# Kernel optimization log

Hardware: AMD Instinct MI355X
Metric: run time of the kernel (lower is better)

## Reference

```python
import jax, jax.numpy as jnp
import numpy as np

B, N, E, H, F, L, S = 4, 384, 768, 32, 3072, 12, 512
D = E // H


def setup_inputs() -> dict:
    key = jax.random.key(0)
    ks = jax.random.split(key, 32)
    inp = {}
    # forward args
    inp['node_type'] = jax.random.randint(ks[0], (B, N, 1), 1, S + 1)  # table has S+1 rows; 0 = pad (unused)
    inp['node_input_feature'] = jax.random.normal(ks[1], (B, N, E), jnp.float32)
    inp['in_degree'] = jax.random.randint(ks[2], (B, N), 0, S)
    inp['out_degree'] = jax.random.randint(ks[3], (B, N), 0, S)
    inp['attn_bias'] = jax.random.normal(ks[4], (B, N, N), jnp.float32) * 0.1
    inp['spatial_pos'] = jax.random.randint(ks[5], (B, N, N), 0, S)
    # embedding tables (normal stddev 0.02, as in the flax module)
    inp['node_emb'] = jax.random.normal(ks[6], (S + 1, E), jnp.float32) * 0.02
    inp['in_deg_emb'] = jax.random.normal(ks[7], (S, E), jnp.float32) * 0.02
    inp['out_deg_emb'] = jax.random.normal(ks[8], (S, E), jnp.float32) * 0.02
    inp['sp_emb'] = jax.random.normal(ks[9], (S, H), jnp.float32) * 0.02
    inp['sp_emb_rev'] = jax.random.normal(ks[10], (S, H), jnp.float32) * 0.02
    # per-layer weights, stacked along leading L axis
    se, sf = 1.0 / np.sqrt(E), 1.0 / np.sqrt(F)
    inp['Wq'] = jax.random.normal(ks[11], (L, E, E), jnp.float32) * se
    inp['bq'] = jax.random.normal(ks[12], (L, E), jnp.float32) * se
    inp['Wk'] = jax.random.normal(ks[13], (L, E, E), jnp.float32) * se
    inp['bk'] = jax.random.normal(ks[14], (L, E), jnp.float32) * se
    inp['Wv'] = jax.random.normal(ks[15], (L, E, E), jnp.float32) * se
    inp['bv'] = jax.random.normal(ks[16], (L, E), jnp.float32) * se
    inp['Wo'] = jax.random.normal(ks[17], (L, E, E), jnp.float32) * se
    inp['bo'] = jnp.zeros((L, E), jnp.float32)
    inp['W1'] = jax.random.normal(ks[18], (L, E, F), jnp.float32) * se
    inp['b1'] = jax.random.normal(ks[19], (L, F), jnp.float32) * se
    inp['W2'] = jax.random.normal(ks[20], (L, F, E), jnp.float32) * sf
    inp['b2'] = jax.random.normal(ks[21], (L, E), jnp.float32) * sf
    inp['ln1_s'] = jnp.ones((L, E), jnp.float32)
    inp['ln1_b'] = jnp.zeros((L, E), jnp.float32)
    inp['ln2_s'] = jnp.ones((L, E), jnp.float32)
    inp['ln2_b'] = jnp.zeros((L, E), jnp.float32)
    return inp


def _layernorm(x, scale, bias, eps=1e-5):
    m = x.mean(-1, keepdims=True)
    v = ((x - m) ** 2).mean(-1, keepdims=True)
    return (x - m) / jnp.sqrt(v + eps) * scale + bias


def _encoder(node_type, node_input_feature, in_degree, out_degree, attn_bias, spatial_pos,
             node_emb, in_deg_emb, out_deg_emb, sp_emb, sp_emb_rev,
             Wq, bq, Wk, bk, Wv, bv, Wo, bo, W1, b1, W2, b2, ln1_s, ln1_b, ln2_s, ln2_b):
    nt = node_type[..., 0]                               # [B,N]
    padding_mask = nt == 0                               # [B,N]
    # node features: node_emb(node_type).sum(-2) + degree embeddings + input feature
    x = (node_emb[node_type].sum(axis=-2)
         + in_deg_emb[in_degree] + out_deg_emb[out_degree]
         + node_input_feature)                           # [B,N,E]
    # spatial attention bias: [B,N,N,H] -> [B,H,N,N], plus graph-level attn_bias
    sb = sp_emb[spatial_pos] + sp_emb_rev[jnp.transpose(spatial_pos, (0, 2, 1))]
    bias = jnp.transpose(sb, (0, 3, 1, 2)) + attn_bias[:, None]  # [B,H,N,N]

    x = jnp.transpose(x, (1, 0, 2))                      # [N,B,E]
    scaling = D ** (-0.5)
    neg_inf = jnp.float32(-jnp.inf)

    def layer(x, p):
        wq, bq_, wk, bk_, wv, bv_, wo, bo_, w1, b1_, w2, b2_, s1, t1, s2, t2 = p
        q = ((x @ wq) + bq_) * scaling                   # [N,B,E], bias scaled too (faithful)
        k = (x @ wk) + bk_
        v = (x @ wv) + bv_
        q = q.reshape(N, B, H, D)
        k = k.reshape(N, B, H, D)
        v = v.reshape(N, B, H, D)
        w = jnp.einsum('nbhd,mbhd->bhnm', q, k) + bias   # [B,H,N,N]
        w = jnp.where(padding_mask[:, None, None, :], neg_inf, w)
        probs = jax.nn.softmax(w.astype(jnp.float32), axis=-1).astype(x.dtype)
        a = jnp.einsum('bhnm,mbhd->nbhd', probs, v).reshape(N, B, E)
        a = a @ wo + bo_
        x = _layernorm(x + a, s1, t1)                    # post-LN
        h = jax.nn.gelu(x @ w1 + b1_)                    # approximate gelu (flax default)
        h = h @ w2 + b2_
        x = _layernorm(x + h, s2, t2)
        return x, None

    xs = (Wq, bq, Wk, bk, Wv, bv, Wo, bo, W1, b1, W2, b2, ln1_s, ln1_b, ln2_s, ln2_b)
    x, _ = jax.lax.scan(layer, x, xs)
    return x                                             # [N,B,E]


def reference(node_type, node_input_feature, in_degree, out_degree, attn_bias, spatial_pos,
              node_emb, in_deg_emb, out_deg_emb, sp_emb, sp_emb_rev,
              Wq, bq, Wk, bk, Wv, bv, Wo, bo, W1, b1, W2, b2, ln1_s, ln1_b, ln2_s, ln2_b):
    return _encoder(node_type, node_input_feature, in_degree, out_degree, attn_bias, spatial_pos,
                    node_emb, in_deg_emb, out_deg_emb, sp_emb, sp_emb_rev,
                    Wq, bq, Wk, bk, Wv, bv, Wo, bo, W1, b1, W2, b2, ln1_s, ln1_b, ln2_s, ln2_b)
```

## Files before the change

kernel.cpp:

```cpp
#include <hip/hip_runtime.h>
#include <hip/hip_bf16.h>

#define Bb 4
#define Nn 384
#define Ee 768
#define Hh 32
#define Ff 3072
#define Ll 12
#define Ss 512
#define Mm (Nn*Bb)

typedef __attribute__((ext_vector_type(8))) short bf16x8;
typedef __attribute__((ext_vector_type(4))) float f32x4;
typedef unsigned short u16;

__device__ __forceinline__ u16 f2b(float f) {
  union { float f; unsigned int i; } c; c.f = f;
  unsigned int x = c.i;
  return (u16)((x + 0x7fffu + ((x >> 16) & 1u)) >> 16);
}
__device__ __forceinline__ float b2f(u16 u) {
  union { unsigned int i; float f; } c; c.i = ((unsigned int)u) << 16; return c.f;
}
__device__ __forceinline__ unsigned pkcvt(float lo, float hi) {
  unsigned r;
  asm("v_cvt_pk_bf16_f32 %0, %1, %2" : "=v"(r) : "v"(lo), "v"(hi));
  return r;
}
__device__ __forceinline__ void gload_lds16(const void* g, void* l) {
  __builtin_amdgcn_global_load_lds((__attribute__((address_space(1))) void*)(g),
                                   (__attribute__((address_space(3))) void*)(l), 16, 0, 0);
}

__global__ __launch_bounds__(256) void embed_kernel(
    const int* __restrict__ node_type, const float* __restrict__ nif,
    const int* __restrict__ in_deg, const int* __restrict__ out_deg,
    const float* __restrict__ node_emb, const float* __restrict__ ind_emb,
    const float* __restrict__ outd_emb,
    float* __restrict__ x, u16* __restrict__ xb)
{
  const int r = blockIdx.x;
  const int n = r / Bb, b = r % Bb;
  const int nt  = node_type[b*Nn + n];
  const int idg = in_deg[b*Nn + n];
  const int odg = out_deg[b*Nn + n];
  for (int c = threadIdx.x; c < Ee; c += 256) {
    float val = node_emb[(size_t)nt*Ee + c] + ind_emb[(size_t)idg*Ee + c]
              + outd_emb[(size_t)odg*Ee + c] + nif[((size_t)b*Nn + n)*Ee + c];
    x[(size_t)r*Ee + c] = val;
    xb[(size_t)r*Ee + c] = f2b(val);
  }
}

__global__ void spT_kernel(const int* __restrict__ sp, int* __restrict__ spT)
{
  __shared__ int tile[32][33];
  const int b = blockIdx.z;
  const int n0 = blockIdx.y * 32, m0 = blockIdx.x * 32;
  const int tx = threadIdx.x, ty = threadIdx.y;
  for (int i = ty; i < 32; i += 8)
    tile[i][tx] = sp[((size_t)b*Nn + n0 + i)*Nn + m0 + tx];
  __syncthreads();
  for (int i = ty; i < 32; i += 8)
    spT[((size_t)b*Nn + m0 + i)*Nn + n0 + tx] = tile[tx][i];
}

__global__ __launch_bounds__(256) void bias_pre_kernel(
    const float* __restrict__ atb, const int* __restrict__ sp, const int* __restrict__ spT,
    const float* __restrict__ sp_emb, const float* __restrict__ sp_emb_rev,
    u16* __restrict__ biasb)
{
  __shared__ float spc[512], sprc[512];
  const int bx = blockIdx.x, h = blockIdx.y, b = blockIdx.z;
  const int t = threadIdx.x;
  for (int i = t; i < 512; i += 256) {
    spc[i]  = sp_emb[(size_t)i*Hh + h];
    sprc[i] = sp_emb_rev[(size_t)i*Hh + h];
  }
  __syncthreads();
  const int q = bx*16 + ((t >> 2) & 15);
  const size_t rowb = ((size_t)b*Nn + q)*Nn;
  u16* outb = biasb + (((size_t)(b*Hh + h)*24 + bx)*24)*256 + t;
  const int mbase = ((t >> 6) << 2) + (t & 3);
  for (int tt = 0; tt < 24; ++tt) {
    const int m = tt*16 + mbase;
    float v = atb[rowb + m] + spc[sp[rowb + m]] + sprc[spT[rowb + m]];
    outb[tt*256] = f2b(v);
  }
}

__global__ __launch_bounds__(256) void wconv_kernel(
    const float* __restrict__ Wq, const float* __restrict__ Wk, const float* __restrict__ Wv,
    const float* __restrict__ Wo, const float* __restrict__ W1, const float* __restrict__ W2,
    int layer0, u16* __restrict__ wTall, unsigned slotStride)
{
  __shared__ float tile[64][65];
  const int layer = layer0 + blockIdx.y;
  u16* slot = wTall + (size_t)blockIdx.y * slotStride;
  int tid = blockIdx.x;
  const float* src; u16* dst; int Ns, Ks;
  if (tid < 432)       { int seg = tid / 144; tid -= seg*144;
                         src = (seg==0?Wq:(seg==1?Wk:Wv)) + (size_t)layer*Ee*Ee;
                         dst = slot + (size_t)seg*589824; Ns = 768; Ks = 768; }
  else if (tid < 576)  { tid -= 432; src = Wo + (size_t)layer*Ee*Ee; dst = slot + 1769472; Ns = 768;  Ks = 768; }
  else if (tid < 1152) { tid -= 576; src = W1 + (size_t)layer*Ee*Ff; dst = slot + 2359296; Ns = 3072; Ks = 768; }
  else                 { tid -= 1152; src = W2 + (size_t)layer*Ff*Ee; dst = slot + 4718592; Ns = 768; Ks = 3072; }
  const int tc = Ns >> 6;
  const int tk = tid / tc, tn = tid % tc;
  const int t = threadIdx.x;
  #pragma unroll
  for (int i = 0; i < 4; ++i) {
    const int id = t + i*256;
    const int r = id >> 4, c = (id & 15) << 2;
    float4 v = *(const float4*)(src + (size_t)(tk*64 + r)*Ns + tn*64 + c);
    tile[r][c+0] = v.x; tile[r][c+1] = v.y; tile[r][c+2] = v.z; tile[r][c+3] = v.w;
  }
  __syncthreads();
  #pragma unroll
  for (int i = 0; i < 2; ++i) {
    const int ch = t + i*256;
    const int n = ch >> 3, kc = (ch & 7) << 3;
    uint4 u;
    u.x = pkcvt(tile[kc+0][n], tile[kc+1][n]);
    u.y = pkcvt(tile[kc+2][n], tile[kc+3][n]);
    u.z = pkcvt(tile[kc+4][n], tile[kc+5][n]);
    u.w = pkcvt(tile[kc+6][n], tile[kc+7][n]);
    *(uint4*)(dst + (size_t)(tn*64 + n)*Ks + tk*64 + kc) = u;
  }
}

template<int EPI>
__global__ __launch_bounds__(256) void gemm3_kernel(
    const u16* __restrict__ A, const u16* __restrict__ Bw,
    const float* __restrict__ b0, const float* __restrict__ b1, const float* __restrict__ b2,
    int Kfull, int Kc, float scaleQ,
    float* __restrict__ outF, u16* __restrict__ outB)
{
  __shared__ __align__(16) u16 As[2][128][64];
  __shared__ __align__(16) u16 Bs[2][64][64];
  const int t = threadIdx.x, lane = t & 63, wave = t >> 6;
  int bx = blockIdx.x, by = blockIdx.y;
  {
    const int gx = gridDim.x;
    const int nwg = gx * gridDim.y;
    const int bid = bx + gx * by;
    const int cpx = nwg >> 3;
    const int s = (bid & 7) * cpx + (bid >> 3);
    bx = s % gx; by = s / gx;
  }
  const int m0 = bx * 128, n0 = by * 64;
  const int k0 = blockIdx.z * Kc;
  const int wm = wave >> 1, wn = wave & 1;
  const int ql = lane & 15, hi = lane >> 4;
  const int nk = Kc >> 6;
  const int sr = t >> 3;
  const int sslot = (t & 7) ^ (sr & 7);
  const size_t aoff = (size_t)(m0 + sr)*Kfull + k0 + (sslot << 3);
  const size_t boff = (size_t)(n0 + sr)*Kfull + k0 + (sslot << 3);
  const size_t rstep = (size_t)32 * Kfull;

  int aro[4][2], bro[2][2];
  #pragma unroll
  for (int ks = 0; ks < 2; ++ks) {
    const int kb = (((ks<<2) + hi) ^ (ql & 7)) << 4;
    #pragma unroll
    for (int f = 0; f < 4; ++f) aro[f][ks] = (wm*64 + f*16 + ql)*128 + kb;
    #pragma unroll
    for (int f = 0; f < 2; ++f) bro[f][ks] = (wn*32 + f*16 + ql)*128 + kb;
  }

  f32x4 acc[4][2];
  #pragma unroll
  for (int a = 0; a < 4; ++a)
    #pragma unroll
    for (int c = 0; c < 2; ++c) acc[a][c] = (f32x4){0.f,0.f,0.f,0.f};

  #pragma unroll
  for (int i = 0; i < 4; ++i)
    gload_lds16(A + aoff + i*rstep, (char*)&As[0][0][0] + i*4096 + t*16);
  #pragma unroll
  for (int i = 0; i < 2; ++i)
    gload_lds16(Bw + boff + i*rstep, (char*)&Bs[0][0][0] + i*4096 + t*16);

  for (int kt = 0; kt < nk; ++kt) {
    const int cur = kt & 1, nxt = cur ^ 1;
    const bool pre = (kt + 1 < nk);
    if (pre) {
      const size_t kk = (size_t)(kt + 1) << 6;
      #pragma unroll
      for (int i = 0; i < 4; ++i)
        gload_lds16(A + aoff + kk + i*rstep, (char*)&As[nxt][0][0] + i*4096 + t*16);
      #pragma unroll
      for (int i = 0; i < 2; ++i)
        gload_lds16(Bw + boff + kk + i*rstep, (char*)&Bs[nxt][0][0] + i*4096 + t*16);
      asm volatile("s_waitcnt vmcnt(6)" ::: "memory");
    } else {
      asm volatile("s_waitcnt vmcnt(0)" ::: "memory");
    }
    __builtin_amdgcn_s_barrier();
    __builtin_amdgcn_sched_barrier(0);

    const char* aBase = (const char*)&As[cur][0][0];
    const char* bBase = (const char*)&Bs[cur][0][0];
    bf16x8 af[4][2], bf[2][2];
    #pragma unroll
    for (int f = 0; f < 4; ++f)
      #pragma unroll
      for (int ks = 0; ks < 2; ++ks)
        af[f][ks] = *(const bf16x8*)(aBase + aro[f][ks]);
    #pragma unroll
    for (int f = 0; f < 2; ++f)
      #pragma unroll
      for (int ks = 0; ks < 2; ++ks)
        bf[f][ks] = *(const bf16x8*)(bBase + bro[f][ks]);
    #pragma unroll
    for (int ks = 0; ks < 2; ++ks)
      #pragma unroll
      for (int fm = 0; fm < 4; ++fm)
        #pragma unroll
        for (int fn = 0; fn < 2; ++fn)
          acc[fm][fn] = __builtin_amdgcn_mfma_f32_16x16x32_bf16(af[fm][ks], bf[fn][ks], acc[fm][fn], 0, 0, 0);
    if (pre) {
      __builtin_amdgcn_sched_barrier(0);
      __builtin_amdgcn_s_barrier();
    }
  }

  #pragma unroll
  for (int fm = 0; fm < 4; ++fm) {
    const int rowb = m0 + wm*64 + fm*16 + hi*4;
    #pragma unroll
    for (int fn = 0; fn < 2; ++fn) {
      const int gcol = n0 + wn*32 + fn*16 + ql;
      float bv, scale = 1.0f;
      if (EPI == 0) {
        const int seg = gcol / 768;
        const int cw = gcol - seg*768;
        bv = (seg == 0) ? b0[cw] : ((seg == 1) ? b1[cw] : b2[cw]);
        if (seg == 0) scale = scaleQ;
      } else if (EPI == 1) {
        bv = (blockIdx.z == 0) ? b0[gcol] : 0.0f;
      } else {
        bv = b0[gcol];
      }
      f32x4 v = acc[fm][fn];
      #pragma unroll
      for (int j = 0; j < 4; ++j) {
        float val = (v[j] + bv) * scale;
        if (EPI == 0) {
          outB[(size_t)(rowb + j) * 2304 + gcol] = f2b(val);
        } else if (EPI == 1) {
          outF[(size_t)blockIdx.z * (Mm*768) + (size_t)(rowb + j) * 768 + gcol] = val;
        } else {
          float arg = 0.7978845608028654f * (val + 0.044715f * val * val * val);
          float e = __expf(2.0f * arg);
          float g = 0.5f * val * (2.0f - 2.0f / (e + 1.0f));
          outB[(size_t)(rowb + j) * 3072 + gcol] = f2b(g);
        }
      }
    }
  }
}

template<int PREBIAS>
__global__ __launch_bounds__(256) void attn2_kernel(
    const u16* __restrict__ qkv,
    const u16* __restrict__ biasb,
    const float* __restrict__ atb, const int* __restrict__ sp, const int* __restrict__ spT,
    const float* __restrict__ sp_emb, const float* __restrict__ sp_emb_rev,
    u16* __restrict__ ab)
{
  __shared__ __align__(16) u16 Kt[384][32];
  __shared__ __align__(16) u16 Vt[32][392];
  __shared__ __align__(16) u16 Qt[64][32];
  __shared__ __align__(16) u16 Pw[4][16][32];
  __shared__ float spc[512], sprc[512];
  const int bid = blockIdx.x;
  const int pair = bid % 3;
  const int h = (bid / 3) % Hh;
  const int b = bid / (3 * Hh);
  const int t = threadIdx.x, lane = t & 63, wave = t >> 6;
  const int ql = lane & 15, hi = lane >> 4;

  for (int idx = t; idx < 384*6; idx += 256) {
    const int m = idx / 6, c = idx - m*6;
    const u16* base = qkv + ((size_t)m*Bb + b)*2304 + h*24 + c*4;
    uint2 kk = *(const uint2*)(base + 768);
    uint2 vv = *(const uint2*)(base + 1536);
    *(uint2*)&Kt[m][c*4] = kk;
    Vt[c*4+0][m] = (u16)(vv.x & 0xffffu); Vt[c*4+1][m] = (u16)(vv.x >> 16);
    Vt[c*4+2][m] = (u16)(vv.y & 0xffffu); Vt[c*4+3][m] = (u16)(vv.y >> 16);
  }
  for (int idx = t; idx < 384*2; idx += 256)
    *(uint2*)&Kt[idx>>1][24 + (idx&1)*4] = make_uint2(0u, 0u);
  for (int idx = t; idx < 8*196; idx += 256)
    *(unsigned*)((char*)&Vt[24][0] + idx*4) = 0u;
  if (!PREBIAS) {
    for (int i = t; i < 512; i += 256) {
      spc[i]  = sp_emb[(size_t)i*Hh + h];
      sprc[i] = sp_emb_rev[(size_t)i*Hh + h];
    }
  }

  for (int qi = 0; qi < 2; ++qi) {
    const int ntile = pair*2 + qi;
    for (int idx = t; idx < 64*6; idx += 256) {
      const int qr = idx / 6, c = idx - qr*6;
      const u16* base = qkv + ((size_t)(ntile*64 + qr)*Bb + b)*2304 + h*24 + c*4;
      *(uint2*)&Qt[qr][c*4] = *(const uint2*)base;
    }
    for (int idx = t; idx < 64*2; idx += 256)
      *(uint2*)&Qt[idx>>1][24 + (idx&1)*4] = make_uint2(0u, 0u);
    __syncthreads();

    const int q0 = ntile*64 + wave*16;
    const int q = q0 + ql;
    const bf16x8 qf = *(const bf16x8*)&Qt[wave*16 + ql][hi*8];

    f32x4 f[24];
    const u16* bp = biasb + (((size_t)(b*Hh + h)*24 + ntile*4 + wave)*24)*256 + lane*4;
    const size_t crow = ((size_t)b*Nn + q)*Nn;
    #pragma unroll
    for (int tt = 0; tt < 24; ++tt) {
      bf16x8 kf = *(const bf16x8*)&Kt[tt*16 + ql][hi*8];
      f32x4 z = (f32x4){0.f,0.f,0.f,0.f};
      f32x4 s = __builtin_amdgcn_mfma_f32_16x16x32_bf16(kf, qf, z, 0, 0, 0);
      if (PREBIAS) {
        uint2 bb = *(const uint2*)(bp + tt*256);
        s[0] += b2f((u16)(bb.x & 0xffffu)); s[1] += b2f((u16)(bb.x >> 16));
        s[2] += b2f((u16)(bb.y & 0xffffu)); s[3] += b2f((u16)(bb.y >> 16));
      } else {
        const int off = tt*16 + hi*4;
        int4 s4 = *(const int4*)(sp + crow + off);
        int4 t4 = *(const int4*)(spT + crow + off);
        float4 a4 = *(const float4*)(atb + crow + off);
        s[0] += a4.x + spc[s4.x] + sprc[t4.x];
        s[1] += a4.y + spc[s4.y] + sprc[t4.y];
        s[2] += a4.z + spc[s4.z] + sprc[t4.z];
        s[3] += a4.w + spc[s4.w] + sprc[t4.w];
      }
      f[tt] = s;
    }

    float mx = -3.0e38f;
    #pragma unroll
    for (int tt = 0; tt < 24; ++tt)
      mx = fmaxf(mx, fmaxf(fmaxf(f[tt][0], f[tt][1]), fmaxf(f[tt][2], f[tt][3])));
    mx = fmaxf(mx, __shfl_xor(mx, 16, 64));
    mx = fmaxf(mx, __shfl_xor(mx, 32, 64));
    float sum = 0.f;
    #pragma unroll
    for (int tt = 0; tt < 24; ++tt) {
      #pragma unroll
      for (int j = 0; j < 4; ++j) { f[tt][j] = __expf(f[tt][j] - mx); sum += f[tt][j]; }
    }
    sum += __shfl_xor(sum, 16, 64);
    sum += __shfl_xor(sum, 32, 64);
    const float inv = 1.0f / sum;

    f32x4 o0 = (f32x4){0.f,0.f,0.f,0.f}, o1 = (f32x4){0.f,0.f,0.f,0.f};
    char* prow = (char*)&Pw[wave][ql][0];
    const int swz = (ql & 3) << 4;
    #pragma unroll
    for (int c = 0; c < 12; ++c) {
      unsigned w0 = pkcvt(f[2*c][0],   f[2*c][1]);
      unsigned w1 = pkcvt(f[2*c][2],   f[2*c][3]);
      unsigned w2 = pkcvt(f[2*c+1][0], f[2*c+1][1]);
      unsigned w3 = pkcvt(f[2*c+1][2], f[2*c+1][3]);
      *(unsigned*)(prow + (((hi*8)      ) ^ swz)) = w0;
      *(unsigned*)(prow + (((hi*8) +  4) ^ swz)) = w1;
      *(unsigned*)(prow + (((hi*8) + 32) ^ swz)) = w2;
      *(unsigned*)(prow + (((hi*8) + 36) ^ swz)) = w3;
      bf16x8 a = *(const bf16x8*)(prow + ((hi*16) ^ swz));
      bf16x8 v0 = *(const bf16x8*)&Vt[ql][c*32 + hi*8];
      bf16x8 v1 = *(const bf16x8*)&Vt[16 + ql][c*32 + hi*8];
      o0 = __builtin_amdgcn_mfma_f32_16x16x32_bf16(a, v0, o0, 0, 0, 0);
      o1 = __builtin_amdgcn_mfma_f32_16x16x32_bf16(a, v1, o1, 0, 0, 0);
    }

    #pragma unroll
    for (int j = 0; j < 4; ++j) {
      float invj = __shfl(inv, hi*4 + j, 64);
      const int qg = q0 + hi*4 + j;
      u16* orow = ab + ((size_t)qg*Bb + b)*Ee + h*24;
      orow[ql] = f2b(o0[j] * invj);
      if (ql < 8) orow[16 + ql] = f2b(o1[j] * invj);
    }
    __syncthreads();
  }
}

template<int NP>
__global__ __launch_bounds__(256) void ln_kernel(
    const float* __restrict__ xin, const float* __restrict__ delta,
    const float* __restrict__ gamma, const float* __restrict__ beta,
    float* __restrict__ xout, u16* __restrict__ xb)
{
  __shared__ float red[8];
  const int r = blockIdx.x, t = threadIdx.x;
  const size_t base = (size_t)r * Ee;
  float v[3];
  #pragma unroll
  for (int i = 0; i < 3; ++i) {
    int c = t + i*256;
    float d = xin[base + c];
    #pragma unroll
    for (int p = 0; p < NP; ++p) d += delta[(size_t)p*(Mm*768) + base + c];
    v[i] = d;
  }
  float s = v[0] + v[1] + v[2];
  #pragma unroll
  for (int off = 1; off < 64; off <<= 1) s += __shfl_xor(s, off, 64);
  if ((t & 63) == 0) red[t >> 6] = s;
  __syncthreads();
  const float mean = (red[0] + red[1] + red[2] + red[3]) * (1.0f / 768.0f);
  float qs = 0.f;
  #pragma unroll
  for (int i = 0; i < 3; ++i) { float d = v[i] - mean; qs += d * d; }
  #pragma unroll
  for (int off = 1; off < 64; off <<= 1) qs += __shfl_xor(qs, off, 64);
  if ((t & 63) == 0) red[4 + (t >> 6)] = qs;
  __syncthreads();
  const float var = (red[4] + red[5] + red[6] + red[7]) * (1.0f / 768.0f);
  const float rstd = rsqrtf(var + 1e-5f);
  #pragma unroll
  for (int i = 0; i < 3; ++i) {
    int c = t + i*256;
    float o = (v[i] - mean) * rstd * gamma[c] + beta[c];
    xout[base + c] = o;
    xb[base + c] = f2b(o);
  }
}

extern "C" void kernel_launch(void* const* d_in, const int* in_sizes, int n_in,
                              void* d_out, int out_size, void* d_ws, size_t ws_size,
                              hipStream_t stream) {
  const int*   node_type  = (const int*)d_in[0];
  const float* nif        = (const float*)d_in[1];
  const int*   in_deg     = (const int*)d_in[2];
  const int*   out_deg    = (const int*)d_in[3];
  const float* atb        = (const float*)d_in[4];
  const int*   sp         = (const int*)d_in[5];
  const float* node_emb   = (const float*)d_in[6];
  const float* ind_emb    = (const float*)d_in[7];
  const float* outd_emb   = (const float*)d_in[8];
  const float* sp_emb     = (const float*)d_in[9];
  const float* sp_emb_rev = (const float*)d_in[10];
  const float* Wq = (const float*)d_in[11]; const float* bq = (const float*)d_in[12];
  const float* Wk = (const float*)d_in[13]; const float* bk = (const float*)d_in[14];
  const float* Wv = (const float*)d_in[15]; const float* bv = (const float*)d_in[16];
  const float* Wo = (const float*)d_in[17]; const float* bo = (const float*)d_in[18];
  const float* W1 = (const float*)d_in[19]; const float* b1 = (const float*)d_in[20];
  const float* W2 = (const float*)d_in[21]; const float* b2 = (const float*)d_in[22];
  const float* ln1s = (const float*)d_in[23]; const float* ln1b = (const float*)d_in[24];
  const float* ln2s = (const float*)d_in[25]; const float* ln2b = (const float*)d_in[26];

  char* ws = (char*)d_ws;
  float* x      = (float*)(ws);
  u16*   xb     = (u16*)(ws +  4718592);
  u16*   qkvb16 = (u16*)(ws +  7077888);
  u16*   abuf   = (u16*)(ws + 14155776);
  u16*   hb     = (u16*)(ws + 16515072);
  float* obufP  = (float*)(ws + 25952256);
  int*   spTb   = (int*)(ws + 44826624);
  u16*   biasb  = (u16*)(ws + 47185920);
  const bool useBias = ws_size >= 99090432ull;
  const bool allW    = ws_size >= 254803968ull;
  u16* wTall = (u16*)(ws + (useBias ? 84934656 : 47185920));
  const unsigned LSLOT = 7077888u;

  embed_kernel<<<Mm, 256, 0, stream>>>(node_type, nif, in_deg, out_deg,
                                       node_emb, ind_emb, outd_emb, x, xb);
  spT_kernel<<<dim3(12, 12, 4), dim3(32, 8), 0, stream>>>(sp, spTb);
  if (useBias)
    bias_pre_kernel<<<dim3(24, 32, 4), 256, 0, stream>>>(atb, sp, spTb, sp_emb, sp_emb_rev, biasb);
  if (allW)
    wconv_kernel<<<dim3(1728, 12), 256, 0, stream>>>(Wq, Wk, Wv, Wo, W1, W2,
                                                     0, wTall, LSLOT);

  const float scaleQ = 0.2041241452319315f;

  for (int l = 0; l < Ll; ++l) {
    const float *bql = bq + (size_t)l*Ee, *bkl = bk + (size_t)l*Ee, *bvl = bv + (size_t)l*Ee;
    const float *bol = bo + (size_t)l*Ee;
    const float *b1l = b1 + (size_t)l*Ff, *b2l = b2 + (size_t)l*Ee;

    if (!allW)
      wconv_kernel<<<dim3(1728, 1), 256, 0, stream>>>(Wq, Wk, Wv, Wo, W1, W2,
                                                      l, wTall, 0u);
    u16* slot = wTall + (size_t)(allW ? l : 0) * LSLOT;
    const u16* qkvT = slot;
    const u16* woT  = slot + 1769472;
    const u16* w1T  = slot + 2359296;
    const u16* w2T  = slot + 4718592;

    gemm3_kernel<0><<<dim3(12, 36), 256, 0, stream>>>(xb, qkvT, bql, bkl, bvl,
                                                      768, 768, scaleQ, nullptr, qkvb16);
    if (useBias)
      attn2_kernel<1><<<384, 256, 0, stream>>>(qkvb16, biasb, atb, sp, spTb,
                                               sp_emb, sp_emb_rev, abuf);
    else
      attn2_kernel<0><<<384, 256, 0, stream>>>(qkvb16, nullptr, atb, sp, spTb,
                                               sp_emb, sp_emb_rev, abuf);
    gemm3_kernel<1><<<dim3(12, 12, 2), 256, 0, stream>>>(abuf, woT, bol, bol, bol,
                                                         768, 384, 1.0f, obufP, nullptr);
    ln_kernel<2><<<Mm, 256, 0, stream>>>(x, obufP, ln1s + (size_t)l*Ee, ln1b + (size_t)l*Ee, x, xb);
    gemm3_kernel<2><<<dim3(12, 48), 256, 0, stream>>>(xb, w1T, b1l, b1l, b1l,
                                                      768, 768, 1.0f, nullptr, hb);
    gemm3_kernel<1><<<dim3(12, 12, 4), 256, 0, stream>>>(hb, w2T, b2l, b2l, b2l,
                                                         3072, 768, 1.0f, obufP, nullptr);
    float* xdst = (l == Ll - 1) ? (float*)d_out : x;
    ln_kernel<4><<<Mm, 256, 0, stream>>>(x, obufP, ln2s + (size_t)l*Ee, ln2b + (size_t)l*Ee, xdst, xb);
  }
}
```

Measured before the change: 1.347 ms.

## Vectorize bias precompute and layernorm, hoist Q padding, per-layer weight conversion

The bias precompute kernel now reads float4/int4 vectors and writes packed bf16 pairs in place of scalar loads and stores. LayerNorm moves to one wave per row with float4 loads and stores and shuffle-only reductions, which drops the shared-memory barriers. Zeroing of the Q padding columns is hoisted out of the per-tile loop in attention. The all-layers weight conversion path is removed, so weights are always converted per layer into a single slot; this adds a conversion kernel inside the timed loop when the workspace is large enough for the old up-front path.

Result: faster. 1.291 ms (-4.1%).

```diff
diff --git a/kernel.cpp b/kernel.cpp
--- a/kernel.cpp
+++ b/kernel.cpp
@@ -78,25 +78,30 @@
     sprc[i] = sp_emb_rev[(size_t)i*Hh + h];
   }
   __syncthreads();
-  const int q = bx*16 + ((t >> 2) & 15);
-  const size_t rowb = ((size_t)b*Nn + q)*Nn;
-  u16* outb = biasb + (((size_t)(b*Hh + h)*24 + bx)*24)*256 + t;
-  const int mbase = ((t >> 6) << 2) + (t & 3);
-  for (int tt = 0; tt < 24; ++tt) {
-    const int m = tt*16 + mbase;
-    float v = atb[rowb + m] + spc[sp[rowb + m]] + sprc[spT[rowb + m]];
-    outb[tt*256] = f2b(v);
+  const int qi = t >> 4;
+  const int ml = (t & 15) << 2;
+  const size_t rowb = ((size_t)b*Nn + bx*16 + qi)*Nn;
+  u16* outb = biasb + ((size_t)(b*Hh + h)*24 + bx)*24*256;
+  #pragma unroll
+  for (int mg = 0; mg < 6; ++mg) {
+    const int m = mg*64 + ml;
+    float4 a4 = *(const float4*)(atb + rowb + m);
+    int4  s4 = *(const int4*)(sp  + rowb + m);
+    int4  t4 = *(const int4*)(spT + rowb + m);
+    const int tt = m >> 4, hi = (m >> 2) & 3;
+    uint2 u;
+    u.x = pkcvt(a4.x + spc[s4.x] + sprc[t4.x], a4.y + spc[s4.y] + sprc[t4.y]);
+    u.y = pkcvt(a4.z + spc[s4.z] + sprc[t4.z], a4.w + spc[s4.w] + sprc[t4.w]);
+    *(uint2*)(outb + tt*256 + hi*64 + qi*4) = u;
   }
 }
 
 __global__ __launch_bounds__(256) void wconv_kernel(
     const float* __restrict__ Wq, const float* __restrict__ Wk, const float* __restrict__ Wv,
     const float* __restrict__ Wo, const float* __restrict__ W1, const float* __restrict__ W2,
-    int layer0, u16* __restrict__ wTall, unsigned slotStride)
+    int layer, u16* __restrict__ slot)
 {
   __shared__ float tile[64][65];
-  const int layer = layer0 + blockIdx.y;
-  u16* slot = wTall + (size_t)blockIdx.y * slotStride;
   int tid = blockIdx.x;
   const float* src; u16* dst; int Ns, Ks;
   if (tid < 432)       { int seg = tid / 144; tid -= seg*144;
@@ -295,6 +300,8 @@
     *(uint2*)&Kt[idx>>1][24 + (idx&1)*4] = make_uint2(0u, 0u);
   for (int idx = t; idx < 8*196; idx += 256)
     *(unsigned*)((char*)&Vt[24][0] + idx*4) = 0u;
+  for (int idx = t; idx < 64*2; idx += 256)
+    *(uint2*)&Qt[idx>>1][24 + (idx&1)*4] = make_uint2(0u, 0u);
   if (!PREBIAS) {
     for (int i = t; i < 512; i += 256) {
       spc[i]  = sp_emb[(size_t)i*Hh + h];
@@ -309,8 +316,6 @@
       const u16* base = qkv + ((size_t)(ntile*64 + qr)*Bb + b)*2304 + h*24 + c*4;
       *(uint2*)&Qt[qr][c*4] = *(const uint2*)base;
     }
-    for (int idx = t; idx < 64*2; idx += 256)
-      *(uint2*)&Qt[idx>>1][24 + (idx&1)*4] = make_uint2(0u, 0u);
     __syncthreads();
 
     const int q0 = ntile*64 + wave*16;
@@ -396,39 +401,54 @@
     const float* __restrict__ gamma, const float* __restrict__ beta,
     float* __restrict__ xout, u16* __restrict__ xb)
 {
-  __shared__ float red[8];
-  const int r = blockIdx.x, t = threadIdx.x;
+  const int wave = threadIdx.x >> 6, lane = threadIdx.x & 63;
+  const int r = blockIdx.x * 4 + wave;
   const size_t base = (size_t)r * Ee;
-  float v[3];
+  const int c0 = lane * 12;
+  float v[12];
   #pragma unroll
   for (int i = 0; i < 3; ++i) {
-    int c = t + i*256;
-    float d = xin[base + c];
-    #pragma unroll
-    for (int p = 0; p < NP; ++p) d += delta[(size_t)p*(Mm*768) + base + c];
-    v[i] = d;
-  }
-  float s = v[0] + v[1] + v[2];
+    float4 xv = *(const float4*)(xin + base + c0 + i*4);
+    v[i*4+0] = xv.x; v[i*4+1] = xv.y; v[i*4+2] = xv.z; v[i*4+3] = xv.w;
+  }
+  #pragma unroll
+  for (int p = 0; p < NP; ++p) {
+    const float* dp = delta + (size_t)p*(Mm*768) + base + c0;
+    #pragma unroll
+    for (int i = 0; i < 3; ++i) {
+      float4 dv = *(const float4*)(dp + i*4);
+      v[i*4+0] += dv.x; v[i*4+1] += dv.y; v[i*4+2] += dv.z; v[i*4+3] += dv.w;
+    }
+  }
+  float s = 0.f;
+  #pragma unroll
+  for (int i = 0; i < 12; ++i) s += v[i];
   #pragma unroll
   for (int off = 1; off < 64; off <<= 1) s += __shfl_xor(s, off, 64);
-  if ((t & 63) == 0) red[t >> 6] = s;
-  __syncthreads();
-  const float mean = (red[0] + red[1] + red[2] + red[3]) * (1.0f / 768.0f);
+  const float mean = s * (1.0f / 768.0f);
   float qs = 0.f;
   #pragma unroll
-  for (int i = 0; i < 3; ++i) { float d = v[i] - mean; qs += d * d; }
+  for (int i = 0; i < 12; ++i) { float d = v[i] - mean; qs += d * d; }
   #pragma unroll
   for (int off = 1; off < 64; off <<= 1) qs += __shfl_xor(qs, off, 64);
-  if ((t & 63) == 0) red[4 + (t >> 6)] = qs;
-  __syncthreads();
-  const float var = (red[4] + red[5] + red[6] + red[7]) * (1.0f / 768.0f);
-  const float rstd = rsqrtf(var + 1e-5f);
+  const float rstd = rsqrtf(qs * (1.0f / 768.0f) + 1e-5f);
+  float o[12];
   #pragma unroll
   for (int i = 0; i < 3; ++i) {
-    int c = t + i*256;
-    float o = (v[i] - mean) * rstd * gamma[c] + beta[c];
-    xout[base + c] = o;
-    xb[base + c] = f2b(o);
+    float4 g4 = *(const float4*)(gamma + c0 + i*4);
+    float4 b4 = *(const float4*)(beta + c0 + i*4);
+    o[i*4+0] = (v[i*4+0] - mean) * rstd * g4.x + b4.x;
+    o[i*4+1] = (v[i*4+1] - mean) * rstd * g4.y + b4.y;
+    o[i*4+2] = (v[i*4+2] - mean) * rstd * g4.z + b4.z;
+    o[i*4+3] = (v[i*4+3] - mean) * rstd * g4.w + b4.w;
+    *(float4*)(xout + base + c0 + i*4) = make_float4(o[i*4+0], o[i*4+1], o[i*4+2], o[i*4+3]);
+  }
+  #pragma unroll
+  for (int i = 0; i < 3; ++i) {
+    uint2 u;
+    u.x = pkcvt(o[i*4+0], o[i*4+1]);
+    u.y = pkcvt(o[i*4+2], o[i*4+3]);
+    *(uint2*)(xb + base + c0 + i*4) = u;
   }
 }
 
@@ -464,19 +484,14 @@
   float* obufP  = (float*)(ws + 25952256);
   int*   spTb   = (int*)(ws + 44826624);
   u16*   biasb  = (u16*)(ws + 47185920);
+  u16*   wTslot = (u16*)(ws + 84934656);
   const bool useBias = ws_size >= 99090432ull;
-  const bool allW    = ws_size >= 254803968ull;
-  u16* wTall = (u16*)(ws + (useBias ? 84934656 : 47185920));
-  const unsigned LSLOT = 7077888u;
 
   embed_kernel<<<Mm, 256, 0, stream>>>(node_type, nif, in_deg, out_deg,
                                        node_emb, ind_emb, outd_emb, x, xb);
   spT_kernel<<<dim3(12, 12, 4), dim3(32, 8), 0, stream>>>(sp, spTb);
   if (useBias)
     bias_pre_kernel<<<dim3(24, 32, 4), 256, 0, stream>>>(atb, sp, spTb, sp_emb, sp_emb_rev, biasb);
-  if (allW)
-    wconv_kernel<<<dim3(1728, 12), 256, 0, stream>>>(Wq, Wk, Wv, Wo, W1, W2,
-                                                     0, wTall, LSLOT);
 
   const float scaleQ = 0.2041241452319315f;
 
@@ -485,14 +500,11 @@
     const float *bol = bo + (size_t)l*Ee;
     const float *b1l = b1 + (size_t)l*Ff, *b2l = b2 + (size_t)l*Ee;
 
-    if (!allW)
-      wconv_kernel<<<dim3(1728, 1), 256, 0, stream>>>(Wq, Wk, Wv, Wo, W1, W2,
-                                                      l, wTall, 0u);
-    u16* slot = wTall + (size_t)(allW ? l : 0) * LSLOT;
-    const u16* qkvT = slot;
-    const u16* woT  = slot + 1769472;
-    const u16* w1T  = slot + 2359296;
-    const u16* w2T  = slot + 4718592;
+    wconv_kernel<<<1728, 256, 0, stream>>>(Wq, Wk, Wv, Wo, W1, W2, l, wTslot);
+    const u16* qkvT = wTslot;
+    const u16* woT  = wTslot + 1769472;
+    const u16* w1T  = wTslot + 2359296;
+    const u16* w2T  = wTslot + 4718592;
 
     gemm3_kernel<0><<<dim3(12, 36), 256, 0, stream>>>(xb, qkvT, bql, bkl, bvl,
                                                       768, 768, scaleQ, nullptr, qkvb16);
@@ -504,12 +516,12 @@
                                                sp_emb, sp_emb_rev, abuf);
     gemm3_kernel<1><<<dim3(12, 12, 2), 256, 0, stream>>>(abuf, woT, bol, bol, bol,
                                                          768, 384, 1.0f, obufP, nullptr);
-    ln_kernel<2><<<Mm, 256, 0, stream>>>(x, obufP, ln1s + (size_t)l*Ee, ln1b + (size_t)l*Ee, x, xb);
+    ln_kernel<2><<<Mm/4, 256, 0, stream>>>(x, obufP, ln1s + (size_t)l*Ee, ln1b + (size_t)l*Ee, x, xb);
     gemm3_kernel<2><<<dim3(12, 48), 256, 0, stream>>>(xb, w1T, b1l, b1l, b1l,
                                                       768, 768, 1.0f, nullptr, hb);
     gemm3_kernel<1><<<dim3(12, 12, 4), 256, 0, stream>>>(hb, w2T, b2l, b2l, b2l,
                                                          3072, 768, 1.0f, obufP, nullptr);
     float* xdst = (l == Ll - 1) ? (float*)d_out : x;
-    ln_kernel<4><<<Mm, 256, 0, stream>>>(x, obufP, ln2s + (size_t)l*Ee, ln2b + (size_t)l*Ee, xdst, xb);
-  }
-}
+    ln_kernel<4><<<Mm/4, 256, 0, stream>>>(x, obufP, ln2s + (size_t)l*Ee, ln2b + (size_t)l*Ee, xdst, xb);
+  }
+}
```
